# Kernel tuning notes

Measured on AMD Instinct MI355X. Metric: run time of the kernel, lower is better.

Reference implementation:

```python
import jax, jax.numpy as jnp
import numpy as np

N_HEADS = 16
NEG_INF = float('-inf')


def setup_inputs() -> dict:
    key = jax.random.key(0)
    ks = jax.random.split(key, 8)
    B, S, D = 8, 1024, 1024
    inp = {
        'q': jax.random.normal(ks[0], (B, S, D), jnp.float32),
        'k': jax.random.normal(ks[1], (B, S, D), jnp.float32),
        'v': jax.random.normal(ks[2], (B, S, D), jnp.float32),
        'key_padding_mask': jnp.zeros((B, S), bool),
        'Wq': jax.random.normal(ks[3], (D, D), jnp.float32) / np.sqrt(D),
        'bq': jnp.zeros((D,), jnp.float32),
        'Wk': jax.random.normal(ks[4], (D, D), jnp.float32) / np.sqrt(D),
        'bk': jnp.zeros((D,), jnp.float32),
        'Wv': jax.random.normal(ks[5], (D, D), jnp.float32) / np.sqrt(D),
        'bv': jnp.zeros((D,), jnp.float32),
        'Wo': jax.random.normal(ks[6], (D, D), jnp.float32) / np.sqrt(D),
        'bo': jnp.zeros((D,), jnp.float32),
    }
    return inp


def reference(q, k, v, key_padding_mask, Wq, bq, Wk, bk, Wv, bv, Wo, bo):
    B, T, D = q.shape
    S = k.shape[1]
    H = N_HEADS
    dh = D // H
    causal = True

    # projections (torch Linear: x @ W.T + b)
    qh = (q @ Wq.T + bq).reshape(B, T, H, dh).transpose(0, 2, 1, 3)  # b h t d
    kh = (k @ Wk.T + bk).reshape(B, S, H, dh).transpose(0, 2, 1, 3)  # b h s d
    vh = (v @ Wv.T + bv).reshape(B, S, H, dh).transpose(0, 2, 1, 3)  # b h s d

    s = jnp.einsum('bhtd,bhsd->bhts', qh, kh) / jnp.sqrt(jnp.asarray(dh, s_dtype(qh)))
    s = jnp.where(key_padding_mask[:, None, None, :], NEG_INF, s)
    if causal:
        cmask = jnp.triu(jnp.full((T, S), NEG_INF, s.dtype), 1)
        s = s + cmask[None, None]
    a = jax.nn.softmax(s.astype(jnp.float32), axis=-1).astype(s.dtype)
    o = jnp.einsum('bhts,bhsd->bhtd', a, vh)
    o = o.transpose(0, 2, 1, 3).reshape(B, T, D)
    return o @ Wo.T + bo


def s_dtype(x):
    return x.dtype
```

## Files before the change

kernel.cpp:

```cpp
#include <hip/hip_runtime.h>
#include <hip/hip_bf16.h>

typedef unsigned short u16;
typedef unsigned int u32;
typedef __attribute__((ext_vector_type(8))) short bf16x8;
typedef __attribute__((ext_vector_type(4))) float f32x4;

#define LOG2E 1.44269504088896340736f
#define QSCALE (0.125f * LOG2E)
#define DEFER_THR 8.0f


__device__ inline u16 f2bf(float f) {
  union { float f; u32 u; } v; v.f = f;
  u32 r = v.u + 0x7fffu + ((v.u >> 16) & 1u);
  return (u16)(r >> 16);
}

__device__ inline void gload_lds16(const void* g, void* l) {
  __builtin_amdgcn_global_load_lds(
      (const __attribute__((address_space(1))) u32*)g,
      (__attribute__((address_space(3))) u32*)l, 16, 0, 0);
}

template<int CTRL>
__device__ inline float dppmov(float x) {
  int i = __builtin_bit_cast(int, x);
  int r = __builtin_amdgcn_update_dpp(i, i, CTRL, 0xf, 0xf, false);
  return __builtin_bit_cast(float, r);
}
__device__ inline float rowmax16(float v) {
  v = fmaxf(v, dppmov<0x128>(v));
  v = fmaxf(v, dppmov<0x124>(v));
  v = fmaxf(v, dppmov<0x122>(v));
  v = fmaxf(v, dppmov<0x121>(v));
  return v;
}
__device__ inline float rowsum16(float v) {
  v += dppmov<0x128>(v);
  v += dppmov<0x124>(v);
  v += dppmov<0x122>(v);
  v += dppmov<0x121>(v);
  return v;
}


__global__ void cvt_multi(const float4* __restrict__ s0, const float4* __restrict__ s1,
                          const float4* __restrict__ s2, const float4* __restrict__ s3,
                          ushort4* __restrict__ d0, ushort4* __restrict__ d1,
                          ushort4* __restrict__ d2, ushort4* __restrict__ d3, int n4) {
  const float4* s; ushort4* d;
  switch (blockIdx.y) {
    case 0: s = s0; d = d0; break;
    case 1: s = s1; d = d1; break;
    case 2: s = s2; d = d2; break;
    default: s = s3; d = d3; break;
  }
  int stride = gridDim.x * blockDim.x;
  for (int i = blockIdx.x * blockDim.x + threadIdx.x; i < n4; i += stride) {
    float4 v = s[i];
    ushort4 o;
    o.x = f2bf(v.x); o.y = f2bf(v.y); o.z = f2bf(v.z); o.w = f2bf(v.w);
    d[i] = o;
  }
}


__global__ void mask_flags(const unsigned char* __restrict__ mask,
                           unsigned char* __restrict__ flags) {
  int t = threadIdx.x;
  if (t >= 128) return;
  const uint4* p = (const uint4*)(mask + (size_t)t * 64);
  uint4 a = p[0], b = p[1], c = p[2], d = p[3];
  u32 v = a.x | a.y | a.z | a.w | b.x | b.y | b.z | b.w |
          c.x | c.y | c.z | c.w | d.x | d.y | d.z | d.w;
  flags[t] = v ? 1 : 0;
}


__global__ __launch_bounds__(256) void gemm_qkv(
    const u16* __restrict__ Aq, const u16* __restrict__ Ak, const u16* __restrict__ Av,
    const u16* __restrict__ Wqb, const u16* __restrict__ Wkb, const u16* __restrict__ Wvb,
    const float* __restrict__ bqp, const float* __restrict__ bkp, const float* __restrict__ bvp,
    u16* __restrict__ Qh, u16* __restrict__ Kh, u16* __restrict__ Vt,
    int M, int N, int K) {
  constexpr int BK = 32;
  __shared__ u16 sA[2][128 * BK];
  __shared__ u16 sB[2][128 * BK];

  const int hw = blockIdx.z * 512 + blockIdx.y * 8 + blockIdx.x;
  const int lg = (hw & 7) * 192 + (hw >> 3);
  const int z = lg / 512;
  const int rem = lg - z * 512;
  const int m0 = (rem >> 3) * 128;
  const int n0 = (rem & 7) * 128;

  const u16* A  = (z == 0) ? Aq : (z == 1) ? Ak : Av;
  const u16* Bt = (z == 0) ? Wqb : (z == 1) ? Wkb : Wvb;
  const float* bias = (z == 0) ? bqp : (z == 1) ? bkp : bvp;

  const int tid = threadIdx.x;
  const int lane = tid & 63;
  const int wave = tid >> 6;
  const int g = lane >> 4;
  const int r = lane & 15;
  const int wr = wave >> 1, wc = wave & 1;

  f32x4 acc[4][4] = {};

  auto stage = [&](int buf, int kt) {
    const int k0 = kt * BK;
#pragma unroll
    for (int i = 0; i < 2; ++i) {
      int c = tid + i * 256;
      int row = c >> 2, cc = c & 3;
      gload_lds16(A + (size_t)(m0 + row) * K + k0 + cc * 8, &sA[buf][0] + c * 8);
    }
#pragma unroll
    for (int i = 0; i < 2; ++i) {
      int c = tid + i * 256;
      int row = c >> 2, cc = c & 3;
      gload_lds16(Bt + (size_t)(n0 + row) * K + k0 + cc * 8, &sB[buf][0] + c * 8);
    }
  };

  stage(0, 0);
  const int NT = K / BK;
  for (int kt = 0; kt < NT; ++kt) {
    __syncthreads();
    if (kt + 1 < NT) stage((kt + 1) & 1, kt + 1);
    const u16* a_base = &sA[kt & 1][0];
    const u16* b_base = &sB[kt & 1][0];
    bf16x8 avf[4], bvf[4];
#pragma unroll
    for (int i = 0; i < 4; ++i) {
      avf[i] = *(const bf16x8*)(a_base + (wr * 64 + i * 16 + r) * BK + g * 8);
      bvf[i] = *(const bf16x8*)(b_base + (wc * 64 + i * 16 + r) * BK + g * 8);
    }
#pragma unroll
    for (int i = 0; i < 4; ++i)
#pragma unroll
      for (int j = 0; j < 4; ++j)
        acc[i][j] = __builtin_amdgcn_mfma_f32_16x16x32_bf16(avf[i], bvf[j], acc[i][j], 0, 0, 0);
  }

#pragma unroll
  for (int i = 0; i < 4; ++i) {
    int rowb = m0 + wr * 64 + i * 16 + g * 4;
#pragma unroll
    for (int j = 0; j < 4; ++j) {
      int col = n0 + wc * 64 + j * 16 + r;
      float bv = bias[col];
#pragma unroll
      for (int q = 0; q < 4; ++q) {
        int row = rowb + q;
        float v = acc[i][j][q] + bv;
        int b = row >> 10, t = row & 1023, h = col >> 6, d = col & 63;
        if (z == 0) {
          Qh[((((size_t)b * 16 + h) << 10) + t) * 64 + d] = f2bf(v * QSCALE);
        } else if (z == 1) {
          Kh[((((size_t)b * 16 + h) << 10) + t) * 64 + d] = f2bf(v);
        } else {
          Vt[(((size_t)b * 16 + h) * 64 + d) * 1024 + t] = f2bf(v);
        }
      }
    }
  }
}


__global__ __launch_bounds__(256) void gemm_o(
    const u16* __restrict__ A, const u16* __restrict__ Bt,
    const float* __restrict__ bias, float* __restrict__ Cout,
    int M, int N, int K) {
  constexpr int BK = 32;
  __shared__ u16 sA[2][128 * BK];
  __shared__ u16 sB[2][128 * BK];

  const int hw = blockIdx.y * 8 + blockIdx.x;
  const int lg = (hw & 7) * 64 + (hw >> 3);
  const int m0 = (lg >> 3) * 128;
  const int n0 = (lg & 7) * 128;

  const int tid = threadIdx.x;
  const int lane = tid & 63;
  const int wave = tid >> 6;
  const int g = lane >> 4;
  const int r = lane & 15;
  const int wr = wave >> 1, wc = wave & 1;

  f32x4 acc[4][4] = {};

  auto stage = [&](int buf, int kt) {
    const int k0 = kt * BK;
#pragma unroll
    for (int i = 0; i < 2; ++i) {
      int c = tid + i * 256;
      int row = c >> 2, cc = c & 3;
      gload_lds16(A + (size_t)(m0 + row) * K + k0 + cc * 8, &sA[buf][0] + c * 8);
    }
#pragma unroll
    for (int i = 0; i < 2; ++i) {
      int c = tid + i * 256;
      int row = c >> 2, cc = c & 3;
      gload_lds16(Bt + (size_t)(n0 + row) * K + k0 + cc * 8, &sB[buf][0] + c * 8);
    }
  };

  stage(0, 0);
  const int NT = K / BK;
  for (int kt = 0; kt < NT; ++kt) {
    __syncthreads();
    if (kt + 1 < NT) stage((kt + 1) & 1, kt + 1);
    const u16* a_base = &sA[kt & 1][0];
    const u16* b_base = &sB[kt & 1][0];
    bf16x8 avf[4], bvf[4];
#pragma unroll
    for (int i = 0; i < 4; ++i) {
      avf[i] = *(const bf16x8*)(a_base + (wr * 64 + i * 16 + r) * BK + g * 8);
      bvf[i] = *(const bf16x8*)(b_base + (wc * 64 + i * 16 + r) * BK + g * 8);
    }
#pragma unroll
    for (int i = 0; i < 4; ++i)
#pragma unroll
      for (int j = 0; j < 4; ++j)
        acc[i][j] = __builtin_amdgcn_mfma_f32_16x16x32_bf16(avf[i], bvf[j], acc[i][j], 0, 0, 0);
  }

#pragma unroll
  for (int i = 0; i < 4; ++i) {
    int rowb = m0 + wr * 64 + i * 16 + g * 4;
#pragma unroll
    for (int j = 0; j < 4; ++j) {
      int col = n0 + wc * 64 + j * 16 + r;
      float bv = bias[col];
#pragma unroll
      for (int q = 0; q < 4; ++q) {
        int row = rowb + q;
        Cout[(size_t)row * N + col] = acc[i][j][q] + bv;
      }
    }
  }
}


__global__ __launch_bounds__(256) void attn_fwd(
    const u16* __restrict__ Qh, const u16* __restrict__ Kh,
    const u16* __restrict__ Vt, const unsigned char* __restrict__ mask,
    const unsigned char* __restrict__ padflags,
    u16* __restrict__ O) {
  constexpr int S = 1024, DH = 64;
  __shared__ u16 sK[2][64 * 64];
  __shared__ u16 sV[2][64 * 64];
  __shared__ u16 sP[4][16 * 64];

  const int tid = threadIdx.x, lane = tid & 63, wave = tid >> 6;
  const int g = lane >> 4, r = lane & 15;
  const int bh = blockIdx.x;
  const int qt = (int)gridDim.y - 1 - (int)blockIdx.y;
  const int b = bh >> 4, h = bh & 15;
  const int qw = qt * 128 + wave * 32;

  bf16x8 qf[2][2];
#pragma unroll
  for (int u = 0; u < 2; ++u) {
    const u16* Qb = Qh + ((size_t)bh * S + qw + u * 16 + r) * DH;
    qf[u][0] = *(const bf16x8*)(Qb + g * 8);
    qf[u][1] = *(const bf16x8*)(Qb + 32 + g * 8);
  }

  f32x4 acc[2][4] = {};
  float mrun[2][4], lrun[2][4];
#pragma unroll
  for (int u = 0; u < 2; ++u)
#pragma unroll
    for (int i = 0; i < 4; ++i) { mrun[u][i] = -INFINITY; lrun[u][i] = 0.f; }

  auto stage = [&](int buf, int kvt) {
    const int s0k = kvt * 64;
#pragma unroll
    for (int i = 0; i < 2; ++i) {
      int c = tid + i * 256;
      int row = c >> 3;
      int cc = (c & 7) ^ (row & 7);
      gload_lds16(Kh + ((size_t)bh * S + s0k + row) * DH + cc * 8, &sK[buf][0] + c * 8);
      gload_lds16(Vt + ((size_t)bh * DH + row) * S + s0k + cc * 8, &sV[buf][0] + c * 8);
    }
  };

  const int NT = 2 * (qt + 1);
  stage(0, 0);
  for (int kvt = 0; kvt < NT; ++kvt) {
    __syncthreads();
    if (kvt + 1 < NT) stage((kvt + 1) & 1, kvt + 1);
    const int cur = kvt & 1;
    const int s0 = kvt * 64;
    const bool pad = padflags[b * 16 + (s0 >> 6)] != 0;
    const u16* Kb = &sK[cur][0];
    const u16* Vb = &sV[cur][0];
    u16* Pw = &sP[wave][0];

#pragma unroll
    for (int u = 0; u < 2; ++u) {
      const int qg = qw + u * 16;
      if (s0 > qg + 15) continue;
      const bool diag = (s0 + 63 > qg);

      f32x4 sc[4] = {};
      __builtin_amdgcn_s_setprio(1);
#pragma unroll
      for (int ss = 0; ss < 4; ++ss) {
#pragma unroll
        for (int kc = 0; kc < 2; ++kc) {
          int krow = ss * 16 + r;
          int byteoff = krow * 128 + kc * 64 + g * 16;
          bf16x8 kf = *(const bf16x8*)((const char*)Kb + (byteoff ^ ((krow & 7) << 4)));
          sc[ss] = __builtin_amdgcn_mfma_f32_16x16x32_bf16(qf[u][kc], kf, sc[ss], 0, 0, 0);
        }
      }
      __builtin_amdgcn_s_setprio(0);

      float sv[4][4];
      float pmax[4] = {-INFINITY, -INFINITY, -INFINITY, -INFINITY};
#pragma unroll
      for (int ss = 0; ss < 4; ++ss) {
        float padd = 0.f;
        if (pad) {
          int s_g = s0 + ss * 16 + r;
          if (mask[(size_t)b * S + s_g]) padd = -INFINITY;
        }
#pragma unroll
        for (int reg = 0; reg < 4; ++reg) {
          float v = sc[ss][reg] + padd;
          if (diag) {
            int s_g = s0 + ss * 16 + r;
            int q_g = qg + g * 4 + reg;
            if (s_g > q_g) v = -INFINITY;
          }
          sv[ss][reg] = v;
          pmax[reg] = fmaxf(pmax[reg], v);
        }
      }

      float tm[4];
#pragma unroll
      for (int reg = 0; reg < 4; ++reg) tm[reg] = rowmax16(pmax[reg]);
      float dmax = fmaxf(fmaxf(tm[0] - mrun[u][0], tm[1] - mrun[u][1]),
                         fmaxf(tm[2] - mrun[u][2], tm[3] - mrun[u][3]));
      if (__any(dmax > DEFER_THR)) {
#pragma unroll
        for (int reg = 0; reg < 4; ++reg) {
          float newm = fmaxf(mrun[u][reg], tm[reg]);
          float alpha = (newm == -INFINITY) ? 1.f : exp2f(mrun[u][reg] - newm);
          mrun[u][reg] = newm;
          float rs = 0.f;
#pragma unroll
          for (int ss = 0; ss < 4; ++ss) {
            float p = (newm == -INFINITY) ? 0.f : exp2f(sv[ss][reg] - newm);
            sv[ss][reg] = p;
            rs += p;
          }
          rs = rowsum16(rs);
          lrun[u][reg] = lrun[u][reg] * alpha + rs;
#pragma unroll
          for (int df = 0; df < 4; ++df) acc[u][df][reg] *= alpha;
        }
      } else {
#pragma unroll
        for (int reg = 0; reg < 4; ++reg) {
          float m = mrun[u][reg];
          float rs = 0.f;
#pragma unroll
          for (int ss = 0; ss < 4; ++ss) {
            float p = (m == -INFINITY) ? 0.f : exp2f(sv[ss][reg] - m);
            sv[ss][reg] = p;
            rs += p;
          }
          rs = rowsum16(rs);
          lrun[u][reg] += rs;
        }
      }

#pragma unroll
      for (int ss = 0; ss < 4; ++ss) {
#pragma unroll
        for (int reg = 0; reg < 4; ++reg) {
          int qrow = g * 4 + reg;
          int byteoff = qrow * 128 + (ss * 16 + r) * 2;
          u32 bits = __builtin_bit_cast(u32, sv[ss][reg]);
          *(u16*)((char*)Pw + (byteoff ^ ((qrow & 7) << 4))) = (u16)(bits >> 16);
        }
      }

      __builtin_amdgcn_s_setprio(1);
#pragma unroll
      for (int sc2 = 0; sc2 < 2; ++sc2) {
        int pbyte = r * 128 + sc2 * 64 + g * 16;
        bf16x8 pf = *(const bf16x8*)((const char*)Pw + (pbyte ^ ((r & 7) << 4)));
#pragma unroll
        for (int df = 0; df < 4; ++df) {
          int vrow = df * 16 + r;
          int vbyte = vrow * 128 + sc2 * 64 + g * 16;
          bf16x8 vf = *(const bf16x8*)((const char*)Vb + (vbyte ^ ((vrow & 7) << 4)));
          acc[u][df] = __builtin_amdgcn_mfma_f32_16x16x32_bf16(pf, vf, acc[u][df], 0, 0, 0);
        }
      }
      __builtin_amdgcn_s_setprio(0);
    }
  }

#pragma unroll
  for (int u = 0; u < 2; ++u) {
#pragma unroll
    for (int reg = 0; reg < 4; ++reg) {
      float l = lrun[u][reg];
      float inv = (l > 0.f) ? 1.f / l : 0.f;
      int t = qw + u * 16 + g * 4 + reg;
#pragma unroll
      for (int df = 0; df < 4; ++df) {
        float vo = acc[u][df][reg] * inv;
        O[((size_t)b * 1024 + t) * 1024 + h * 64 + df * 16 + r] = f2bf(vo);
      }
    }
  }
}


extern "C" void kernel_launch(void* const* d_in, const int* in_sizes, int n_in,
                              void* d_out, int out_size, void* d_ws, size_t ws_size,
                              hipStream_t stream) {
  const float* q  = (const float*)d_in[0];
  const float* k  = (const float*)d_in[1];
  const float* v  = (const float*)d_in[2];
  const unsigned char* mask = (const unsigned char*)d_in[3];
  const float* Wq = (const float*)d_in[4];
  const float* bq = (const float*)d_in[5];
  const float* Wk = (const float*)d_in[6];
  const float* bk = (const float*)d_in[7];
  const float* Wv = (const float*)d_in[8];
  const float* bv = (const float*)d_in[9];
  const float* Wo = (const float*)d_in[10];
  const float* bo = (const float*)d_in[11];

  const int M = 8192, N = 1024, K = 1024;
  const size_t MB = 1u << 20;
  char* ws = (char*)d_ws;

  u16* Aq   = (u16*)(ws);
  u16* Ak   = (u16*)(ws + 16 * MB);
  u16* Av   = (u16*)(ws + 32 * MB);
  u16* Qh   = (u16*)(ws + 48 * MB);
  u16* Kh   = (u16*)(ws + 64 * MB);
  u16* Vt   = (u16*)(ws + 80 * MB);
  u16* Wqb  = (u16*)(ws + 96 * MB);
  u16* Wkb  = Wqb + (1u << 20);
  u16* Wvb  = Wkb + (1u << 20);
  u16* Wob  = Wvb + (1u << 20);
  unsigned char* flags = (unsigned char*)(ws + 104 * MB);
  u16* AttO = Aq;

  cvt_multi<<<dim3(1024, 3), 256, 0, stream>>>(
      (const float4*)q, (const float4*)k, (const float4*)v, (const float4*)q,
      (ushort4*)Aq, (ushort4*)Ak, (ushort4*)Av, (ushort4*)Aq, (M * K) / 4);
  cvt_multi<<<dim3(256, 4), 256, 0, stream>>>(
      (const float4*)Wq, (const float4*)Wk, (const float4*)Wv, (const float4*)Wo,
      (ushort4*)Wqb, (ushort4*)Wkb, (ushort4*)Wvb, (ushort4*)Wob, (N * K) / 4);
  mask_flags<<<1, 128, 0, stream>>>(mask, flags);

  gemm_qkv<<<dim3(8, 64, 3), 256, 0, stream>>>(
      Aq, Ak, Av, Wqb, Wkb, Wvb, bq, bk, bv, Qh, Kh, Vt, M, N, K);

  attn_fwd<<<dim3(128, 8), 256, 0, stream>>>(Qh, Kh, Vt, mask, flags, AttO);

  gemm_o<<<dim3(8, 64), 256, 0, stream>>>(
      AttO, Wob, bo, (float*)d_out, M, N, K);
}
```

Baseline: 229.9 us.

## Rewrite QKV GEMM with 256x256 tiles, 8 waves, swizzled LDS and interleaved pipeline

Replaces the 128x128, 4-wave QKV projection GEMM with a 256x256 tile, 512-thread kernel using BK=64. It stages A and B in half-tiles, XOR-swizzles the LDS layout to avoid bank conflicts, and interleaves global-to-LDS loads with the MFMA quadrants, using vmcnt gates and setprio. The goal is more data reuse per tile and better overlap of loads and compute. In exchange it uses more LDS and registers per block and launches fewer blocks, which may lower occupancy and leave CUs idle at the tail.

```diff
diff --git a/kernel.cpp b/kernel.cpp
--- a/kernel.cpp
+++ b/kernel.cpp
@@ -78,22 +78,76 @@
 }
 
 
-__global__ __launch_bounds__(256) void gemm_qkv(
+#define GATE() do { \
+    asm volatile("s_waitcnt vmcnt(4)" ::: "memory"); \
+    __builtin_amdgcn_s_barrier(); \
+    __builtin_amdgcn_sched_barrier(0); \
+  } while (0)
+
+#define READ_A(buf, qm)                                                        \
+  do {                                                                         \
+    const char* base_ = (const char*)&sA[buf][wm][0];                          \
+    _Pragma("unroll")                                                          \
+    for (int fi = 0; fi < 4; ++fi) {                                           \
+      _Pragma("unroll")                                                        \
+      for (int kk = 0; kk < 2; ++kk) {                                         \
+        int row_ = (qm) * 64 + fi * 16 + r;                                    \
+        int j_ = kk * 4 + g;                                                   \
+        af[fi][kk] = *(const bf16x8*)(base_ + row_ * 128 +                     \
+                                      ((j_ ^ (row_ & 7)) << 4));               \
+      }                                                                        \
+    }                                                                          \
+  } while (0)
+
+#define READ_B(buf, qn, BF)                                                    \
+  do {                                                                         \
+    const char* base_ = (const char*)&sB[buf][wn >> 1][0];                     \
+    _Pragma("unroll")                                                          \
+    for (int fj = 0; fj < 2; ++fj) {                                           \
+      _Pragma("unroll")                                                        \
+      for (int kk = 0; kk < 2; ++kk) {                                         \
+        int row_ = (wn & 1) * 64 + (qn) * 32 + fj * 16 + r;                    \
+        int j_ = kk * 4 + g;                                                   \
+        BF[fj][kk] = *(const bf16x8*)(base_ + row_ * 128 +                     \
+                                      ((j_ ^ (row_ & 7)) << 4));               \
+      }                                                                        \
+    }                                                                          \
+  } while (0)
+
+#define MFMA8(qm, qn, BF)                                                      \
+  do {                                                                         \
+    __builtin_amdgcn_s_setprio(1);                                             \
+    _Pragma("unroll")                                                          \
+    for (int kk = 0; kk < 2; ++kk) {                                           \
+      _Pragma("unroll")                                                        \
+      for (int fi = 0; fi < 4; ++fi) {                                         \
+        _Pragma("unroll")                                                      \
+        for (int fj = 0; fj < 2; ++fj) {                                       \
+          acc[(qm) * 4 + fi][(qn) * 2 + fj] =                                  \
+              __builtin_amdgcn_mfma_f32_16x16x32_bf16(                         \
+                  af[fi][kk], BF[fj][kk], acc[(qm) * 4 + fi][(qn) * 2 + fj],   \
+                  0, 0, 0);                                                    \
+        }                                                                      \
+      }                                                                        \
+    }                                                                          \
+    __builtin_amdgcn_s_setprio(0);                                             \
+  } while (0)
+
+__global__ __launch_bounds__(512) void gemm_qkv8(
     const u16* __restrict__ Aq, const u16* __restrict__ Ak, const u16* __restrict__ Av,
     const u16* __restrict__ Wqb, const u16* __restrict__ Wkb, const u16* __restrict__ Wvb,
     const float* __restrict__ bqp, const float* __restrict__ bkp, const float* __restrict__ bvp,
     u16* __restrict__ Qh, u16* __restrict__ Kh, u16* __restrict__ Vt,
     int M, int N, int K) {
-  constexpr int BK = 32;
-  __shared__ u16 sA[2][128 * BK];
-  __shared__ u16 sB[2][128 * BK];
-
-  const int hw = blockIdx.z * 512 + blockIdx.y * 8 + blockIdx.x;
-  const int lg = (hw & 7) * 192 + (hw >> 3);
-  const int z = lg / 512;
-  const int rem = lg - z * 512;
-  const int m0 = (rem >> 3) * 128;
-  const int n0 = (rem & 7) * 128;
+  __shared__ u16 sA[2][2][128 * 64];
+  __shared__ u16 sB[2][2][128 * 64];
+
+  const int hw = blockIdx.z * 128 + blockIdx.y * 4 + blockIdx.x;
+  const int lg = (hw & 7) * 48 + (hw >> 3);
+  const int z = lg >> 7;
+  const int rem = lg & 127;
+  const int m0 = (rem >> 2) * 256;
+  const int n0 = (rem & 3) * 256;
 
   const u16* A  = (z == 0) ? Aq : (z == 1) ? Ak : Av;
   const u16* Bt = (z == 0) ? Wqb : (z == 1) ? Wkb : Wvb;
@@ -104,57 +158,72 @@
   const int wave = tid >> 6;
   const int g = lane >> 4;
   const int r = lane & 15;
-  const int wr = wave >> 1, wc = wave & 1;
-
-  f32x4 acc[4][4] = {};
-
-  auto stage = [&](int buf, int kt) {
-    const int k0 = kt * BK;
+  const int wm = wave >> 2;
+  const int wn = wave & 3;
+
+  f32x4 acc[8][4] = {};
+  bf16x8 af[4][2], bf0[2][2], bf1[2][2];
+
+  auto stageA = [&](int buf, int half, int kt) {
+    const int k0 = kt * 64;
 #pragma unroll
     for (int i = 0; i < 2; ++i) {
-      int c = tid + i * 256;
-      int row = c >> 2, cc = c & 3;
-      gload_lds16(A + (size_t)(m0 + row) * K + k0 + cc * 8, &sA[buf][0] + c * 8);
-    }
+      int c = tid + i * 512;
+      int row = c >> 3, cc = c & 7;
+      gload_lds16(A + (size_t)(m0 + half * 128 + row) * K + k0 + ((cc ^ (row & 7)) * 8),
+                  &sA[buf][half][0] + c * 8);
+    }
+  };
+  auto stageB = [&](int buf, int half, int kt) {
+    const int k0 = kt * 64;
 #pragma unroll
     for (int i = 0; i < 2; ++i) {
-      int c = tid + i * 256;
-      int row = c >> 2, cc = c & 3;
-      gload_lds16(Bt + (size_t)(n0 + row) * K + k0 + cc * 8, &sB[buf][0] + c * 8);
+      int c = tid + i * 512;
+      int row = c >> 3, cc = c & 7;
+      gload_lds16(Bt + (size_t)(n0 + half * 128 + row) * K + k0 + ((cc ^ (row & 7)) * 8),
+                  &sB[buf][half][0] + c * 8);
     }
   };
 
-  stage(0, 0);
-  const int NT = K / BK;
-  for (int kt = 0; kt < NT; ++kt) {
-    __syncthreads();
-    if (kt + 1 < NT) stage((kt + 1) & 1, kt + 1);
-    const u16* a_base = &sA[kt & 1][0];
-    const u16* b_base = &sB[kt & 1][0];
-    bf16x8 avf[4], bvf[4];
-#pragma unroll
-    for (int i = 0; i < 4; ++i) {
-      avf[i] = *(const bf16x8*)(a_base + (wr * 64 + i * 16 + r) * BK + g * 8);
-      bvf[i] = *(const bf16x8*)(b_base + (wc * 64 + i * 16 + r) * BK + g * 8);
-    }
-#pragma unroll
-    for (int i = 0; i < 4; ++i)
-#pragma unroll
-      for (int j = 0; j < 4; ++j)
-        acc[i][j] = __builtin_amdgcn_mfma_f32_16x16x32_bf16(avf[i], bvf[j], acc[i][j], 0, 0, 0);
-  }
-
-#pragma unroll
-  for (int i = 0; i < 4; ++i) {
-    int rowb = m0 + wr * 64 + i * 16 + g * 4;
-#pragma unroll
-    for (int j = 0; j < 4; ++j) {
-      int col = n0 + wc * 64 + j * 16 + r;
+  const int NT = K / 64;
+
+  stageB(0, 0, 0); stageB(0, 1, 0); stageA(0, 0, 0); stageA(0, 1, 0);
+  stageB(1, 0, 1); stageA(1, 0, 1);
+  asm volatile("s_waitcnt vmcnt(0)" ::: "memory");
+  __builtin_amdgcn_s_barrier();
+  __builtin_amdgcn_sched_barrier(0);
+
+  for (int t = 0; t < NT; ++t) {
+    const int buf = t & 1;
+    READ_A(buf, 0);
+    READ_B(buf, 0, bf0);
+    if (t + 1 < NT) stageB(buf ^ 1, 1, t + 1);
+    GATE();
+    MFMA8(0, 0, bf0);
+    READ_B(buf, 1, bf1);
+    if (t + 1 < NT) stageA(buf ^ 1, 1, t + 1);
+    GATE();
+    MFMA8(0, 1, bf1);
+    READ_A(buf, 1);
+    if (t + 2 < NT) stageB(buf, 0, t + 2);
+    GATE();
+    MFMA8(1, 0, bf0);
+    if (t + 2 < NT) stageA(buf, 0, t + 2);
+    GATE();
+    MFMA8(1, 1, bf1);
+  }
+
+#pragma unroll
+  for (int fi = 0; fi < 8; ++fi) {
+    int rowb = m0 + wm * 128 + fi * 16 + g * 4;
+#pragma unroll
+    for (int fj = 0; fj < 4; ++fj) {
+      int col = n0 + wn * 64 + fj * 16 + r;
       float bv = bias[col];
 #pragma unroll
       for (int q = 0; q < 4; ++q) {
         int row = rowb + q;
-        float v = acc[i][j][q] + bv;
+        float v = acc[fi][fj][q] + bv;
         int b = row >> 10, t = row & 1023, h = col >> 6, d = col & 63;
         if (z == 0) {
           Qh[((((size_t)b * 16 + h) << 10) + t) * 64 + d] = f2bf(v * QSCALE);
@@ -467,7 +536,7 @@
       (ushort4*)Wqb, (ushort4*)Wkb, (ushort4*)Wvb, (ushort4*)Wob, (N * K) / 4);
   mask_flags<<<1, 128, 0, stream>>>(mask, flags);
 
-  gemm_qkv<<<dim3(8, 64, 3), 256, 0, stream>>>(
+  gemm_qkv8<<<dim3(4, 32, 3), 512, 0, stream>>>(
       Aq, Ak, Av, Wqb, Wkb, Wvb, bq, bk, bv, Qh, Kh, Vt, M, N, K);
 
   attn_fwd<<<dim3(128, 8), 256, 0, stream>>>(Qh, Kh, Vt, mask, flags, AttO);
```

After: 241.5 us. 1.05x slower.
